# Kernel tuning notes

Measured on AMD Instinct MI355X. Metric: run time of the kernel, lower is better.

The kernel has to match this reference:

```python
import jax, jax.numpy as jnp
import numpy as np
import math

B, T, D = 2, 2048, 1024
H, HD = 16, 64  # n_heads, head_dim; H*HD == D

def setup_inputs() -> dict:
    key = jax.random.key(0)
    ks = jax.random.split(key, 5)
    s = 1.0 / math.sqrt(D)
    return {
        "x": jax.random.normal(ks[0], (B, T, D), dtype=jnp.float32),
        "w_qkv": jax.random.normal(ks[1], (D, 3 * D), dtype=jnp.float32) * s,
        "b_qkv": jax.random.normal(ks[2], (3 * D,), dtype=jnp.float32) * 0.01,
        "w_o": jax.random.normal(ks[3], (D, D), dtype=jnp.float32) * s,
        "b_o": jax.random.normal(ks[4], (D,), dtype=jnp.float32) * 0.01,
    }

def reference(x, w_qkv, b_qkv, w_o, b_o):
    b, t, d_model = x.shape
    qkv = x @ w_qkv + b_qkv                       # [b,t,3d]
    q, k, v = jnp.split(qkv, 3, axis=-1)
    # [b,t,d] -> [b,h,t,hd]
    q = q.reshape(b, t, H, HD).transpose(0, 2, 1, 3)
    k = k.reshape(b, t, H, HD).transpose(0, 2, 1, 3)
    v = v.reshape(b, t, H, HD).transpose(0, 2, 1, 3)
    # NOTE: original scales by sqrt(d_model), not sqrt(head_dim)
    scores = jnp.einsum('bhqd,bhkd->bhqk', q, k) / math.sqrt(d_model)
    causal = jnp.tril(jnp.ones((t, t), dtype=bool))
    scores = jnp.where(causal[None, None], scores, -jnp.inf)
    # dropout p=0.0 (pre-softmax in original) is identity
    attn = jax.nn.softmax(scores, axis=-1)
    y = jnp.einsum('bhqk,bhkd->bhqd', attn, v)    # [b,h,t,hd]
    y = y.transpose(0, 2, 1, 3).reshape(b, t, d_model)
    return y @ w_o + b_o
```

## Files before the change

### kernel.cpp

```cpp
#include <hip/hip_runtime.h>
#include <math.h>

typedef __bf16 bf16;
typedef __bf16 bf16x4 __attribute__((ext_vector_type(4)));
typedef __bf16 bf16x8 __attribute__((ext_vector_type(8)));
typedef float f32x4 __attribute__((ext_vector_type(4)));

__device__ __forceinline__ void async_copy16(const void* g, void* l) {
  __builtin_amdgcn_global_load_lds(
      (__attribute__((address_space(1))) void*)(const_cast<void*>(g)),
      (__attribute__((address_space(3))) void*)(l),
      16, 0, 0);
}

__device__ __forceinline__ void transpose_tile(
    const float* __restrict__ in, bf16* __restrict__ out, int R, int C,
    int bxi, int byi) {
  __shared__ float tile[32][33];
  int bx = bxi * 32, by = byi * 32;
  int tx = threadIdx.x & 31;
  int ty = threadIdx.x >> 5;
#pragma unroll
  for (int i = 0; i < 32; i += 8)
    tile[ty + i][tx] = in[(size_t)(by + ty + i) * C + bx + tx];
  __syncthreads();
#pragma unroll
  for (int i = 0; i < 32; i += 8)
    out[(size_t)(bx + ty + i) * R + by + tx] = (bf16)tile[tx][ty + i];
}

__global__ __launch_bounds__(256) void prep_kernel(
    const float* __restrict__ x, bf16* __restrict__ xb,
    const float* __restrict__ w_qkv, bf16* __restrict__ wqkvT,
    const float* __restrict__ w_o, bf16* __restrict__ woT) {
  int blk = blockIdx.x;
  if (blk < 4096) {
    int i = blk * 1024 + threadIdx.x * 4;
    float4 v = *(const float4*)(x + i);
    bf16x4 o;
    o[0] = (bf16)v.x; o[1] = (bf16)v.y; o[2] = (bf16)v.z; o[3] = (bf16)v.w;
    *(bf16x4*)(xb + i) = o;
  } else if (blk < 7168) {
    int tb = blk - 4096;
    transpose_tile(w_qkv, wqkvT, 1024, 3072, tb % 96, tb / 96);
  } else {
    int tb = blk - 7168;
    transpose_tile(w_o, woT, 1024, 1024, tb % 32, tb / 32);
  }
}

__global__ __launch_bounds__(256) void gemm_qkv_kernel(
    const bf16* __restrict__ A, const bf16* __restrict__ Bt,
    const float* __restrict__ bias, bf16* __restrict__ qb,
    bf16* __restrict__ kb, bf16* __restrict__ vtb) {
  __shared__ bf16 As[64 * 64];
  __shared__ bf16 Bs[128 * 64];
  int bm = blockIdx.x, bn = blockIdx.y;
  int tid = threadIdx.x;
  int w = tid >> 6, lane = tid & 63;
  int wm = w & 1, wn = w >> 1;
  int col = lane & 15, quad = lane >> 4;

  const bf16* Ab = A + (size_t)(bm * 64) * 1024;
  const bf16* Bb = Bt + (size_t)(bn * 128) * 1024;
  f32x4 acc[2][4] = {};

  int lrow = lane >> 3;
  int lch = lane & 7;

  for (int k0 = 0; k0 < 1024; k0 += 64) {
    __syncthreads();
#pragma unroll
    for (int c = 0; c < 2; c++) {
      int r = w * 16 + c * 8 + lrow;
      int ch = lch ^ (r & 7);
      async_copy16(Ab + (size_t)r * 1024 + k0 + ch * 8,
                   As + (w * 16 + c * 8) * 64);
    }
#pragma unroll
    for (int c = 0; c < 4; c++) {
      int r = w * 32 + c * 8 + lrow;
      int ch = lch ^ (r & 7);
      async_copy16(Bb + (size_t)r * 1024 + k0 + ch * 8,
                   Bs + (w * 32 + c * 8) * 64);
    }
    __syncthreads();

#pragma unroll
    for (int ks = 0; ks < 2; ks++) {
      bf16x8 af[2], bfr[4];
#pragma unroll
      for (int mi = 0; mi < 2; mi++) {
        int m = wm * 32 + mi * 16 + col;
        af[mi] =
            *(const bf16x8*)(As + m * 64 + (((ks << 2) + quad) ^ (m & 7)) * 8);
      }
#pragma unroll
      for (int ni = 0; ni < 4; ni++) {
        int n = wn * 64 + ni * 16 + col;
        bfr[ni] =
            *(const bf16x8*)(Bs + n * 64 + (((ks << 2) + quad) ^ (n & 7)) * 8);
      }
#pragma unroll
      for (int mi = 0; mi < 2; mi++)
#pragma unroll
        for (int ni = 0; ni < 4; ni++)
          acc[mi][ni] = __builtin_amdgcn_mfma_f32_16x16x32_bf16(
              bfr[ni], af[mi], acc[mi][ni], 0, 0, 0);
    }
  }

#pragma unroll
  for (int ni = 0; ni < 4; ni++) {
    int f0 = bn * 128 + wn * 64 + ni * 16 + quad * 4;
    float4 b4 = *(const float4*)(bias + f0);
    int which = f0 >> 10;
    int dd = f0 & 1023;
    int h = dd >> 6, hd0 = dd & 63;
    if (which == 2) {
#pragma unroll
      for (int mi = 0; mi < 2; mi++) {
        int tok = bm * 64 + wm * 32 + mi * 16 + col;
        int b = tok >> 11, t = tok & 2047;
        size_t base = ((size_t)(b * 16 + h) * 64 + hd0) * 2048 + t;
        vtb[base] = (bf16)(acc[mi][ni][0] + b4.x);
        vtb[base + 2048] = (bf16)(acc[mi][ni][1] + b4.y);
        vtb[base + 4096] = (bf16)(acc[mi][ni][2] + b4.z);
        vtb[base + 6144] = (bf16)(acc[mi][ni][3] + b4.w);
      }
    } else {
      bf16* dst = (which == 0) ? qb : kb;
#pragma unroll
      for (int mi = 0; mi < 2; mi++) {
        int tok = bm * 64 + wm * 32 + mi * 16 + col;
        int b = tok >> 11, t = tok & 2047;
        bf16x4 pk;
        pk[0] = (bf16)(acc[mi][ni][0] + b4.x);
        pk[1] = (bf16)(acc[mi][ni][1] + b4.y);
        pk[2] = (bf16)(acc[mi][ni][2] + b4.z);
        pk[3] = (bf16)(acc[mi][ni][3] + b4.w);
        *(bf16x4*)&dst[((size_t)(b * 16 + h) * 2048 + t) * 64 + hd0] = pk;
      }
    }
  }
}

__global__ __launch_bounds__(256) void gemm_out_kernel(
    const bf16* __restrict__ A, const bf16* __restrict__ Bt,
    const float* __restrict__ bias, float* __restrict__ outp) {
  __shared__ bf16 As[64 * 64];
  __shared__ bf16 Bs[64 * 64];
  int bm = blockIdx.x, bn = blockIdx.y;
  int tid = threadIdx.x;
  int w = tid >> 6, lane = tid & 63;
  int wm = w & 1, wn = w >> 1;
  int col = lane & 15, quad = lane >> 4;

  const bf16* Ab = A + (size_t)(bm * 64) * 1024;
  const bf16* Bb = Bt + (size_t)(bn * 64) * 1024;
  f32x4 acc[2][2] = {};

  int lrow = lane >> 3;
  int lch = lane & 7;

  for (int k0 = 0; k0 < 1024; k0 += 64) {
    __syncthreads();
#pragma unroll
    for (int c = 0; c < 2; c++) {
      int r = w * 16 + c * 8 + lrow;
      int ch = lch ^ (r & 7);
      async_copy16(Ab + (size_t)r * 1024 + k0 + ch * 8,
                   As + (w * 16 + c * 8) * 64);
      async_copy16(Bb + (size_t)r * 1024 + k0 + ch * 8,
                   Bs + (w * 16 + c * 8) * 64);
    }
    __syncthreads();

#pragma unroll
    for (int ks = 0; ks < 2; ks++) {
      bf16x8 af[2], bfr[2];
#pragma unroll
      for (int mi = 0; mi < 2; mi++) {
        int m = wm * 32 + mi * 16 + col;
        af[mi] =
            *(const bf16x8*)(As + m * 64 + (((ks << 2) + quad) ^ (m & 7)) * 8);
      }
#pragma unroll
      for (int ni = 0; ni < 2; ni++) {
        int n = wn * 32 + ni * 16 + col;
        bfr[ni] =
            *(const bf16x8*)(Bs + n * 64 + (((ks << 2) + quad) ^ (n & 7)) * 8);
      }
#pragma unroll
      for (int mi = 0; mi < 2; mi++)
#pragma unroll
        for (int ni = 0; ni < 2; ni++)
          acc[mi][ni] = __builtin_amdgcn_mfma_f32_16x16x32_bf16(
              bfr[ni], af[mi], acc[mi][ni], 0, 0, 0);
    }
  }

#pragma unroll
  for (int ni = 0; ni < 2; ni++) {
    int f0 = bn * 64 + wn * 32 + ni * 16 + quad * 4;
    float4 b4 = *(const float4*)(bias + f0);
#pragma unroll
    for (int mi = 0; mi < 2; mi++) {
      int tok = bm * 64 + wm * 32 + mi * 16 + col;
      float4 ov;
      ov.x = acc[mi][ni][0] + b4.x;
      ov.y = acc[mi][ni][1] + b4.y;
      ov.z = acc[mi][ni][2] + b4.z;
      ov.w = acc[mi][ni][3] + b4.w;
      *(float4*)(outp + (size_t)tok * 1024 + f0) = ov;
    }
  }
}

__global__ __launch_bounds__(256, 4) void attn_kernel(
    const bf16* __restrict__ qb, const bf16* __restrict__ kb,
    const bf16* __restrict__ vtb, bf16* __restrict__ y) {
  __shared__ bf16 Ks[2][64 * 64];
  __shared__ bf16 Vs[2][64 * 64];
  __shared__ bf16 Pl[4][16][40];

  int idx = blockIdx.x;
  int qp = idx >> 5;
  int qt = (qp < 8) ? 31 - qp
           : (qp < 16) ? qp - 8
           : (qp < 24) ? 39 - qp
                       : qp - 16;
  int bh = idx & 31;
  int b = bh >> 4, h = bh & 15;
  int tid = threadIdx.x, w = tid >> 6, lane = tid & 63;
  int col = lane & 15, quad = lane >> 4;

  const bf16* Qh = qb + (size_t)bh * (2048 * 64);
  const bf16* Kh = kb + (size_t)bh * (2048 * 64);
  const bf16* Vth = vtb + (size_t)bh * (64 * 2048);

  int qrow = qt * 64 + w * 16 + col;
  bf16x8 aq[2];
#pragma unroll
  for (int ks = 0; ks < 2; ks++) {
    aq[ks] = *(const bf16x8*)(Qh + (size_t)qrow * 64 + ks * 32 + quad * 8);
#pragma unroll
    for (int e = 0; e < 8; e++)
      aq[ks][e] = (bf16)((float)aq[ks][e] * 0.03125f);
  }

  int r0 = w * 16 + (lane >> 3);
  int r1 = r0 + 8;
  int ch0 = (lane & 7) ^ (r0 & 7);
  int ch1 = (lane & 7) ^ (r1 & 7);
  size_t koff0 = (size_t)r0 * 64 + ch0 * 8;
  size_t koff1 = (size_t)r1 * 64 + ch1 * 8;
  size_t voff0 = (size_t)r0 * 2048 + ch0 * 8;
  size_t voff1 = (size_t)r1 * 2048 + ch1 * 8;
  int lw0 = (w * 16) * 64;
  int lw1 = (w * 16 + 8) * 64;

  float l_part = 0.f;
  f32x4 ot[4] = {};
  int qglob = qt * 64 + w * 16 + col;

  auto stage = [&](int j, int buf) {
    const bf16* Kt = Kh + (size_t)j * 64 * 64;
    const bf16* Vt_ = Vth + (size_t)j * 64;
    async_copy16(Kt + koff0, Ks[buf] + lw0);
    async_copy16(Kt + koff1, Ks[buf] + lw1);
    async_copy16(Vt_ + voff0, Vs[buf] + lw0);
    async_copy16(Vt_ + voff1, Vs[buf] + lw1);
  };

  auto tile_compute = [&](int j, int buf, bool diag) {
    const bf16* Ksb = Ks[buf];
    const bf16* Vsb = Vs[buf];
    f32x4 st[4] = {};
#pragma unroll
    for (int ks = 0; ks < 2; ks++)
#pragma unroll
      for (int c = 0; c < 4; c++) {
        int t = c * 16 + col;
        int slot = t * 8 + (((ks << 2) + quad) ^ (t & 7));
        bf16x8 ak = *(const bf16x8*)(Ksb + slot * 8);
        st[c] = __builtin_amdgcn_mfma_f32_16x16x32_bf16(ak, aq[ks], st[c],
                                                        0, 0, 0);
      }
#pragma unroll
    for (int half = 0; half < 2; half++) {
#pragma unroll
      for (int cc = 0; cc < 2; cc++) {
        int c = half * 2 + cc;
        bf16x4 pk;
#pragma unroll
        for (int r = 0; r < 4; r++) {
          int tglob = j * 64 + c * 16 + quad * 4 + r;
          float pv = (diag && tglob > qglob) ? 0.f : __expf(st[c][r]);
          l_part += pv;
          pk[r] = (bf16)pv;
        }
        *(bf16x4*)&Pl[w][col][cc * 16 + quad * 4] = pk;
      }
      __builtin_amdgcn_sched_barrier(0);
      __builtin_amdgcn_s_waitcnt(0xc07f);
      __builtin_amdgcn_sched_barrier(0);
      bf16x8 ap = *(const bf16x8*)&Pl[w][col][quad * 8];
#pragma unroll
      for (int c = 0; c < 4; c++) {
        int d = c * 16 + col;
        int slot = d * 8 + (((half << 2) + quad) ^ (d & 7));
        bf16x8 av = *(const bf16x8*)(Vsb + slot * 8);
        ot[c] = __builtin_amdgcn_mfma_f32_16x16x32_bf16(av, ap, ot[c],
                                                        0, 0, 0);
      }
    }
  };

  int j = 0;
  for (; j < qt; j += 2) {
    __syncthreads();
    stage(j, 0);
    stage(j + 1, 1);
    __syncthreads();
    tile_compute(j, 0, false);
    tile_compute(j + 1, 1, j + 1 == qt);
  }
  if (j == qt) {
    __syncthreads();
    stage(j, 0);
    __syncthreads();
    tile_compute(j, 0, true);
  }

  float sum = l_part;
  sum += __shfl_xor(sum, 16, 64);
  sum += __shfl_xor(sum, 32, 64);
  float inv = 1.f / sum;
  int tq = qt * 64 + w * 16 + col;
  bf16* yrow = y + ((size_t)(b * 2048 + tq)) * 1024 + h * 64;
#pragma unroll
  for (int c = 0; c < 4; c++) {
    bf16x4 pk;
#pragma unroll
    for (int r = 0; r < 4; r++) pk[r] = (bf16)(ot[c][r] * inv);
    *(bf16x4*)(yrow + c * 16 + quad * 4) = pk;
  }
}

extern "C" void kernel_launch(void* const* d_in, const int* in_sizes, int n_in,
                              void* d_out, int out_size, void* d_ws,
                              size_t ws_size, hipStream_t stream) {
  const float* x = (const float*)d_in[0];
  const float* w_qkv = (const float*)d_in[1];
  const float* b_qkv = (const float*)d_in[2];
  const float* w_o = (const float*)d_in[3];
  const float* b_o = (const float*)d_in[4];
  float* out = (float*)d_out;

  char* p = (char*)d_ws;
  bf16* xb    = (bf16*)p; p += (size_t)4096 * 1024 * 2;
  bf16* wqkvT = (bf16*)p; p += (size_t)3072 * 1024 * 2;
  bf16* woT   = (bf16*)p; p += (size_t)1024 * 1024 * 2;
  bf16* qb    = (bf16*)p; p += (size_t)2 * 16 * 2048 * 64 * 2;
  bf16* kb    = (bf16*)p; p += (size_t)2 * 16 * 2048 * 64 * 2;
  bf16* vtb   = (bf16*)p; p += (size_t)2 * 16 * 64 * 2048 * 2;
  bf16* yb    = (bf16*)p; p += (size_t)4096 * 1024 * 2;

  prep_kernel<<<8192, 256, 0, stream>>>(x, xb, w_qkv, wqkvT, w_o, woT);
  gemm_qkv_kernel<<<dim3(64, 24), 256, 0, stream>>>(
      xb, wqkvT, b_qkv, qb, kb, vtb);
  attn_kernel<<<1024, 256, 0, stream>>>(qb, kb, vtb, yb);
  gemm_out_kernel<<<dim3(64, 16), 256, 0, stream>>>(yb, woT, b_o, out);
}
```

Measured before the change: 165.2 us.

## Vectorize weight transpose and stage full swizzled P tile per wave

The weight transpose now reads one float4 per thread and writes packed bf16x4, instead of scalar loads and stores. In attention, each wave writes all four 16-column P chunks into a larger XOR-swizzled LDS buffer before a single wait, so the two half-steps no longer each wait on their own write. This cuts LDS wait points and transpose instruction count. The P buffer grows per wave, which raises LDS use and may affect occupancy.

```diff
diff --git a/kernel.cpp b/kernel.cpp
--- a/kernel.cpp
+++ b/kernel.cpp
@@ -18,15 +18,25 @@
     int bxi, int byi) {
   __shared__ float tile[32][33];
   int bx = bxi * 32, by = byi * 32;
-  int tx = threadIdx.x & 31;
-  int ty = threadIdx.x >> 5;
-#pragma unroll
-  for (int i = 0; i < 32; i += 8)
-    tile[ty + i][tx] = in[(size_t)(by + ty + i) * C + bx + tx];
+  int tid = threadIdx.x;
+  {
+    int row = tid >> 3;
+    int cq = tid & 7;
+    float4 v = *(const float4*)(in + (size_t)(by + row) * C + bx + cq * 4);
+    tile[row][cq * 4 + 0] = v.x;
+    tile[row][cq * 4 + 1] = v.y;
+    tile[row][cq * 4 + 2] = v.z;
+    tile[row][cq * 4 + 3] = v.w;
+  }
   __syncthreads();
-#pragma unroll
-  for (int i = 0; i < 32; i += 8)
-    out[(size_t)(bx + ty + i) * R + by + tx] = (bf16)tile[tx][ty + i];
+  {
+    int c = tid >> 3;
+    int rq = tid & 7;
+    bf16x4 pk;
+#pragma unroll
+    for (int e = 0; e < 4; e++) pk[e] = (bf16)tile[rq * 4 + e][c];
+    *(bf16x4*)(out + (size_t)(bx + c) * R + by + rq * 4) = pk;
+  }
 }
 
 __global__ __launch_bounds__(256) void prep_kernel(
@@ -222,7 +232,7 @@
     const bf16* __restrict__ vtb, bf16* __restrict__ y) {
   __shared__ bf16 Ks[2][64 * 64];
   __shared__ bf16 Vs[2][64 * 64];
-  __shared__ bf16 Pl[4][16][40];
+  __shared__ bf16 Pl[4][16 * 64];
 
   int idx = blockIdx.x;
   int qp = idx >> 5;
@@ -264,6 +274,9 @@
   f32x4 ot[4] = {};
   int qglob = qt * 64 + w * 16 + col;
 
+  bf16* PlW = Pl[w];
+  int pq = col & 7;
+
   auto stage = [&](int j, int buf) {
     const bf16* Kt = Kh + (size_t)j * 64 * 64;
     const bf16* Vt_ = Vth + (size_t)j * 64;
@@ -288,24 +301,27 @@
                                                         0, 0, 0);
       }
 #pragma unroll
+    for (int c = 0; c < 4; c++) {
+      bf16x4 pk;
+#pragma unroll
+      for (int r = 0; r < 4; r++) {
+        int tglob = j * 64 + c * 16 + quad * 4 + r;
+        float pv = (diag && tglob > qglob) ? 0.f : __expf(st[c][r]);
+        l_part += pv;
+        pk[r] = (bf16)pv;
+      }
+      int chunk = ((c << 1) + (quad >> 1)) ^ pq;
+      *(bf16x4*)(PlW + col * 64 + chunk * 8 + (quad & 1) * 4) = pk;
+    }
+
+    __builtin_amdgcn_sched_barrier(0);
+    __builtin_amdgcn_s_waitcnt(0xc07f);
+    __builtin_amdgcn_sched_barrier(0);
+
+#pragma unroll
     for (int half = 0; half < 2; half++) {
-#pragma unroll
-      for (int cc = 0; cc < 2; cc++) {
-        int c = half * 2 + cc;
-        bf16x4 pk;
-#pragma unroll
-        for (int r = 0; r < 4; r++) {
-          int tglob = j * 64 + c * 16 + quad * 4 + r;
-          float pv = (diag && tglob > qglob) ? 0.f : __expf(st[c][r]);
-          l_part += pv;
-          pk[r] = (bf16)pv;
-        }
-        *(bf16x4*)&Pl[w][col][cc * 16 + quad * 4] = pk;
-      }
-      __builtin_amdgcn_sched_barrier(0);
-      __builtin_amdgcn_s_waitcnt(0xc07f);
-      __builtin_amdgcn_sched_barrier(0);
-      bf16x8 ap = *(const bf16x8*)&Pl[w][col][quad * 8];
+      int pchunk = ((half << 2) + quad) ^ pq;
+      bf16x8 ap = *(const bf16x8*)(PlW + col * 64 + pchunk * 8);
 #pragma unroll
       for (int c = 0; c < 4; c++) {
         int d = c * 16 + col;
```

New measurement: 163.2 us. Within noise of the previous version (-1.2%).
